# Kernel tuning notes

Hardware: AMD Instinct MI355X
Metric: run time of the kernel (lower is better)

## Reference

```python
import jax, jax.numpy as jnp
import numpy as np

B, N, E, D, N_NODE = 512, 64, 64, 256, 200000
NEG = -9e15
ALPHA = 0.2  # leaky-relu slope from HGNN_ATT(..., 0.2, ...)


def _hgat_layer(x, adj_mask, w2, w3, a, a2, wc, w=None):
    """HyperGraphAttentionLayerSparse (HyperGAT), dense-masked vectorized form.
    x: [B,N,d_in], adj_mask: [B,E,N] bool. Returns (node [B,N,d], edge [B,E,d]).
    Eval mode: dropout is identity. concat=False so no ELU on output."""
    d = w2.shape[1]
    x4 = x @ w2                                            # [B,N,d]
    if w is not None:                                      # transfer=True path
        x = x @ w
    # node->edge attention: score = leakyrelu([word_context; x4_node] @ a), independent of edge idx
    s1 = jax.nn.leaky_relu(jnp.dot(wc, a[:d, 0]) + x4 @ a[d:, 0], ALPHA)   # [B,N]
    att_edge = jax.nn.softmax(jnp.where(adj_mask, s1[:, None, :], NEG), axis=2)  # [B,E,N]
    edge = att_edge @ x                                    # [B,E,d]
    edge4 = edge @ w3                                      # [B,E,d]
    # edge->node attention: score = leakyrelu([x4_node; edge4_edge] @ a2)
    s_pair = jax.nn.leaky_relu((x4 @ a2[:d, 0])[:, None, :] + (edge4 @ a2[d:, 0])[:, :, None], ALPHA)  # [B,E,N]
    att_node = jax.nn.softmax(jnp.swapaxes(jnp.where(adj_mask, s_pair, NEG), 1, 2), axis=2)  # [B,N,E]
    node = att_node @ edge                                 # [B,N,d]
    return node, edge


def setup_inputs() -> dict:
    key = jax.random.key(0)
    ks = jax.random.split(key, 16)
    stdv = 1.0 / np.sqrt(D)  # SessionGraph.reset_parameters uniform(-stdv, stdv)
    u = lambda k, shape: jax.random.uniform(k, shape, jnp.float32, -stdv, stdv)
    return {
        "inputs": jax.random.randint(ks[0], (B, N), 0, N_NODE, dtype=jnp.int32),
        "HT": (jax.random.uniform(ks[1], (B, E, N)) < 0.3).astype(jnp.int32),
        "G": jnp.zeros((1,), jnp.float32),
        "EG": jnp.zeros((1,), jnp.float32),
        "emb_w": u(ks[2], (N_NODE, D)),
        "emb2_w": u(ks[3], (N_NODE, D)),
        "g1_w2": u(ks[4], (D, D)),
        "g1_w3": u(ks[5], (D, D)),
        "g1_a": u(ks[6], (2 * D, 1)),
        "g1_a2": u(ks[7], (2 * D, 1)),
        "g1_wc": u(ks[8], (D,)),
        "g2_w": u(ks[9], (D, D)),
        "g2_w2": u(ks[10], (D, D)),
        "g2_w3": u(ks[11], (D, D)),
        "g2_a": u(ks[12], (2 * D, 1)),
        "g2_a2": u(ks[13], (2 * D, 1)),
        "g2_wc": u(ks[14], (D,)),
    }


def reference(inputs, HT, G, EG, emb_w, emb2_w, g1_w2, g1_w3, g1_a, g1_a2, g1_wc,
              g2_w, g2_w2, g2_w3, g2_a, g2_a2, g2_wc):
    adj_mask = HT > 0
    x = emb_w[inputs]                                      # [B,N,D] embedding gather
    residual = x
    # HGNN_ATT with step=2: gat1 (transfer=False) + residual, gat2 (transfer=True) + residual
    x, _ = _hgat_layer(x, adj_mask, g1_w2, g1_w3, g1_a, g1_a2, g1_wc)
    x = x + residual
    x, _ = _hgat_layer(x, adj_mask, g2_w2, g2_w3, g2_a, g2_a2, g2_wc, g2_w)
    x = x + residual
    nodes2 = emb2_w[inputs]                                # second embedding gather
    return (x, x, nodes2)  # (nodes, hidden, nodes2); hidden aliases nodes in the original
```

## Files before the change

### kernel.cpp

```cpp
#include <hip/hip_runtime.h>

#define BB 512
#define NN 64
#define EE 64
#define DD 256
#define BND (BB * NN * DD)
#define SA 68

typedef __attribute__((ext_vector_type(8))) short s8v;
typedef __attribute__((ext_vector_type(4))) float f4v;
typedef __attribute__((ext_vector_type(8))) unsigned short u16x8;

__device__ __forceinline__ unsigned short f2bf(float f) {
    unsigned int x = __float_as_uint(f);
    x = x + 0x7fffu + ((x >> 16) & 1u);
    return (unsigned short)(x >> 16);
}
__device__ __forceinline__ float bf2f(unsigned short u) {
    return __uint_as_float(((unsigned int)u) << 16);
}
__device__ __forceinline__ float lrelu(float v) { return v > 0.f ? v : 0.2f * v; }

#define WS_PREP  0
#define WS_P3B   8192
#define WS_WFRAG 12288

__global__ void prep_dots(const float* __restrict__ w2a, const float* __restrict__ w3a,
                          const float* __restrict__ aa, const float* __restrict__ a2a,
                          const float* __restrict__ wca,
                          const float* __restrict__ w2b, const float* __restrict__ w3b,
                          const float* __restrict__ ab, const float* __restrict__ a2b,
                          const float* __restrict__ wcb,
                          float* __restrict__ prep, float* __restrict__ p3b_ws) {
    const int t = threadIdx.x;
    const int blk = blockIdx.x;
    const int layer = blk >> 3;
    const int r0 = (blk & 7) * 32;
    __shared__ float vhi[256], v2lo[256], v2hi[256], red[256];
    const float* w2 = layer ? w2b : w2a;
    const float* w3 = layer ? w3b : w3a;
    const float* av = layer ? ab : aa;
    const float* a2 = layer ? a2b : a2a;
    vhi[t] = av[256 + t];
    v2lo[t] = a2[t];
    v2hi[t] = a2[256 + t];
    __syncthreads();
    const int row = r0 + (t >> 3), q = t & 7;
    const float* w2r = w2 + (size_t)row * DD + q * 32;
    const float* w3r = w3 + (size_t)row * DD + q * 32;
    float s1 = 0.f, s2 = 0.f, s3 = 0.f;
    #pragma unroll
    for (int c = 0; c < 8; c++) {
        float4 v = *(const float4*)&w2r[c * 4];
        float4 u = *(const float4*)&w3r[c * 4];
        float4 p1 = *(const float4*)&vhi[q * 32 + c * 4];
        float4 p2 = *(const float4*)&v2lo[q * 32 + c * 4];
        float4 p3 = *(const float4*)&v2hi[q * 32 + c * 4];
        s1 = fmaf(v.x, p1.x, fmaf(v.y, p1.y, fmaf(v.z, p1.z, fmaf(v.w, p1.w, s1))));
        s2 = fmaf(v.x, p2.x, fmaf(v.y, p2.y, fmaf(v.z, p2.z, fmaf(v.w, p2.w, s2))));
        s3 = fmaf(u.x, p3.x, fmaf(u.y, p3.y, fmaf(u.z, p3.z, fmaf(u.w, p3.w, s3))));
    }
    s1 += __shfl_xor(s1, 1); s1 += __shfl_xor(s1, 2); s1 += __shfl_xor(s1, 4);
    s2 += __shfl_xor(s2, 1); s2 += __shfl_xor(s2, 2); s2 += __shfl_xor(s2, 4);
    s3 += __shfl_xor(s3, 1); s3 += __shfl_xor(s3, 2); s3 += __shfl_xor(s3, 4);
    if (q == 0) {
        if (layer == 0) { prep[row] = s1; prep[256 + row] = s2; prep[512 + row] = s3; }
        else { prep[1024 + row] = s1; prep[1280 + row] = s2; p3b_ws[row] = s3; }
    }
    if ((blk & 7) == 0) {
        red[t] = layer ? (wcb[t] * ab[t]) : (wca[t] * aa[t]);
        __syncthreads();
        for (int o = 128; o > 0; o >>= 1) { if (t < o) red[t] += red[t + o]; __syncthreads(); }
        if (t == 0) prep[layer ? 1792 : 768] = red[0];
    }
}

__global__ void prep2_pack(const float* __restrict__ wtr, const float* __restrict__ p3b_ws,
                           float* __restrict__ prep, unsigned short* __restrict__ wfrag) {
    const int t = threadIdx.x, blk = blockIdx.x;
    __shared__ float p3[256];
    if (blk < 8) {
        p3[t] = p3b_ws[t];
        __syncthreads();
        const int row = blk * 32 + (t >> 3), q = t & 7;
        const float* wr = wtr + (size_t)row * DD + q * 32;
        float s = 0.f;
        #pragma unroll
        for (int c = 0; c < 8; c++) {
            float4 v = *(const float4*)&wr[c * 4];
            float4 p = *(const float4*)&p3[q * 32 + c * 4];
            s = fmaf(v.x, p.x, fmaf(v.y, p.y, fmaf(v.z, p.z, fmaf(v.w, p.w, s))));
        }
        s += __shfl_xor(s, 1); s += __shfl_xor(s, 2); s += __shfl_xor(s, 4);
        if (q == 0) prep[1536 + row] = s;
    } else {
        int gid = (blk - 8) * 256 + t;
        int l = gid & 63, frag = gid >> 6;
        int kc = frag >> 4, nt = frag & 15;
        int kb = kc * 32 + (l >> 4) * 8;
        int n = nt * 16 + (l & 15);
        u16x8 u;
        #pragma unroll
        for (int j = 0; j < 8; j++) u[j] = f2bf(wtr[(size_t)(kb + j) * DD + n]);
        *(u16x8*)(wfrag + (size_t)gid * 8) = u;
    }
}

__launch_bounds__(512, 4)
__global__ void mega(const int* __restrict__ inputs, const int* __restrict__ HT,
                     const float* __restrict__ emb_w, const float* __restrict__ emb2_w,
                     const float* __restrict__ prep, const unsigned short* __restrict__ wfrag,
                     float* __restrict__ out) {
    __shared__ unsigned short bufA[256 * SA];
    __shared__ unsigned short RA[64 * SA];
    __shared__ unsigned short RB[64 * SA];
    __shared__ unsigned short RC[64 * SA];
    __shared__ unsigned short RD[64 * SA];
    __shared__ unsigned short XT[16 * SA];
    __shared__ unsigned short pvs[6 * 256];
    __shared__ float dvs[384];
    __shared__ float db2[192];
    __shared__ float u1f[64], invdef[64];
    __shared__ unsigned long long mE[64], mN[64];

    const int b = blockIdx.x;
    const int t = threadIdx.x;
    const int lane = t & 63;
    const int w8 = t >> 6;
    const int l15 = lane & 15, lh = lane >> 4;

    for (int i = t; i < 1536; i += 512) {
        int off = i + (((i >> 8) >= 3) ? 256 : 0);
        pvs[i] = f2bf(prep[off]);
    }
    for (int i = t; i < 16 * SA; i += 512) XT[i] = 0;
    {
        const int rw = t >> 3, q8 = t & 7;
        const int idx = inputs[b * 64 + rw];
        const float* src = emb_w + (size_t)idx * DD + q8 * 32;
        #pragma unroll
        for (int c = 0; c < 8; c++) {
            float4 v = ((const float4*)src)[c];
            ushort4 u;
            u.x = f2bf(v.x); u.y = f2bf(v.y); u.z = f2bf(v.z); u.w = f2bf(v.w);
            *(ushort4*)&bufA[rw * 264 + q8 * 32 + c * 4] = u;
        }
    }
    float4 n2r[8];
    #pragma unroll
    for (int c = 0; c < 8; c++) {
        int i = t + 512 * c;
        int n = i >> 6, cc = i & 63;
        int idx = inputs[b * 64 + n];
        n2r[c] = ((const float4*)(emb2_w + (size_t)idx * DD))[cc];
    }
    #pragma unroll
    for (int i = 0; i < 8; i++) {
        int e = w8 * 8 + i;
        int hx = HT[((size_t)b * EE + e) * NN + lane];
        unsigned long long m = __ballot(hx > 0);
        if (lane == 0) mE[e] = m;
    }
    __syncthreads();

    if (w8 < 4) {
        const int wtile = w8 * 16;
        const int j = (l15 < 6) ? l15 : 5;
        f4v acc = {0.f, 0.f, 0.f, 0.f};
        #pragma unroll
        for (int kc = 0; kc < 8; kc++) {
            s8v a = *(const s8v*)&bufA[(wtile + l15) * 264 + kc * 32 + lh * 8];
            s8v bv = *(const s8v*)&pvs[j * 256 + kc * 32 + lh * 8];
            acc = __builtin_amdgcn_mfma_f32_16x16x32_bf16(a, bv, acc, 0, 0, 0);
        }
        if (l15 < 6) {
            #pragma unroll
            for (int rg = 0; rg < 4; rg++)
                dvs[l15 * 64 + wtile + lh * 4 + rg] = acc[rg];
        }
    } else if (w8 == 4) {
        unsigned long long acc = 0ull;
        for (int e = 0; e < 64; e++) acc |= ((mE[e] >> lane) & 1ull) << e;
        mN[lane] = acc;
    }
    __syncthreads();

    const int wr = (w8 & 3) * 16;
    const int wc = (w8 >> 2) * 32;
    const int row0 = wr + lh * 4;

    {
        float s1l = lrelu(prep[768] + dvs[lane]);
        float g1 = s1l;
        #pragma unroll
        for (int o = 32; o > 0; o >>= 1) g1 = fmaxf(g1, __shfl_xor(g1, o));
        float E1 = __expf(s1l - g1);
        #pragma unroll
        for (int i = 0; i < 8; i++) {
            int e = w8 * 8 + i;
            unsigned long long me = mE[e];
            float pe = (me == 0ull) ? 1.f : (((me >> lane) & 1ull) ? E1 : 0.f);
            unsigned short bf = f2bf(pe);
            RA[lane * SA + e] = bf;
            RC[e * SA + lane] = bf;
        }
    }
    __syncthreads();

    if (w8 < 4) {
        const int etile = w8 * 16;
        f4v acc = {0.f, 0.f, 0.f, 0.f};
        #pragma unroll
        for (int kc = 0; kc < 2; kc++) {
            u16x8 au;
            #pragma unroll
            for (int jj = 0; jj < 8; jj++) {
                int k = kc * 32 + lh * 8 + jj;
                float v = (l15 == 0) ? 1.f : ((l15 <= 4) ? dvs[(l15 + 1) * 64 + k] : 0.f);
                au[jj] = f2bf(v);
            }
            s8v bv = *(const s8v*)&RC[(etile + l15) * SA + kc * 32 + lh * 8];
            acc = __builtin_amdgcn_mfma_f32_16x16x32_bf16((s8v)au, bv, acc, 0, 0, 0);
        }
        int e = etile + l15;
        if (lh == 0) {
            float De = acc[0], We = acc[1];
            invdef[e] = 1.f / De;
            u1f[e] = We / De;
            XT[e] = f2bf(De);
            XT[1 * SA + e] = f2bf(acc[2]);
            XT[2 * SA + e] = f2bf(acc[3]);
        } else if (lh == 1) {
            XT[3 * SA + e] = f2bf(acc[0]);
        }
    }
    __syncthreads();

    {
        float t2l = dvs[64 + lane];
        float gt2 = t2l;
        #pragma unroll
        for (int o = 32; o > 0; o >>= 1) gt2 = fmaxf(gt2, __shfl_xor(gt2, o));
        float um = u1f[lane];
        #pragma unroll
        for (int o = 32; o > 0; o >>= 1) um = fmaxf(um, __shfl_xor(um, o));
        float M1 = lrelu(gt2 + um);
        float ul = u1f[lane];
        float ide = invdef[lane];
        #pragma unroll
        for (int i = 0; i < 8; i++) {
            int n = w8 * 8 + i;
            unsigned long long mn = mN[n];
            float t2n = dvs[64 + n];
            float pr = (mn == 0ull) ? 1.f
                     : (((mn >> lane) & 1ull) ? __expf(lrelu(t2n + ul) - M1) : 0.f);
            RB[n * SA + lane] = f2bf(pr * ide);
        }
    }
    __syncthreads();

    {
        f4v a0 = {0.f,0.f,0.f,0.f}, a1 = {0.f,0.f,0.f,0.f}, ax = {0.f,0.f,0.f,0.f};
        #pragma unroll
        for (int kc = 0; kc < 2; kc++) {
            s8v a  = *(const s8v*)&RB[(wr + l15) * SA + kc * 32 + lh * 8];
            s8v b0 = *(const s8v*)&RA[(wc + l15) * SA + kc * 32 + lh * 8];
            s8v b1 = *(const s8v*)&RA[(wc + 16 + l15) * SA + kc * 32 + lh * 8];
            s8v bx = *(const s8v*)&XT[l15 * SA + kc * 32 + lh * 8];
            a0 = __builtin_amdgcn_mfma_f32_16x16x32_bf16(a, b0, a0, 0, 0, 0);
            a1 = __builtin_amdgcn_mfma_f32_16x16x32_bf16(a, b1, a1, 0, 0, 0);
            ax = __builtin_amdgcn_mfma_f32_16x16x32_bf16(a, bx, ax, 0, 0, 0);
        }
        float invdn[4];
        #pragma unroll
        for (int rg = 0; rg < 4; rg++) invdn[rg] = 1.f / __shfl(ax[rg], lh << 4);
        int col0 = wc + l15, col1 = wc + 16 + l15;
        ushort4 u0, u1;
        #pragma unroll
        for (int rg = 0; rg < 4; rg++) {
            ((unsigned short*)&u0)[rg] = f2bf(a0[rg] * invdn[rg] + ((row0 + rg) == col0 ? 1.f : 0.f));
            ((unsigned short*)&u1)[rg] = f2bf(a1[rg] * invdn[rg] + ((row0 + rg) == col1 ? 1.f : 0.f));
        }
        *(ushort4*)&RD[col0 * SA + row0] = u0;
        *(ushort4*)&RD[col1 * SA + row0] = u1;
        if (w8 < 4 && l15 >= 1 && l15 <= 3) {
            int jj = l15 - 1;
            #pragma unroll
            for (int rg = 0; rg < 4; rg++)
                db2[jj * 64 + row0 + rg] = ax[rg] * invdn[rg] + dvs[(jj + 3) * 64 + row0 + rg];
        }
    }
    __syncthreads();

    {
        float s2l = lrelu(prep[1792] + db2[lane]);
        float g2 = s2l;
        #pragma unroll
        for (int o = 32; o > 0; o >>= 1) g2 = fmaxf(g2, __shfl_xor(g2, o));
        float E2 = __expf(s2l - g2);
        #pragma unroll
        for (int i = 0; i < 8; i++) {
            int e = w8 * 8 + i;
            unsigned long long me = mE[e];
            float pe = (me == 0ull) ? 1.f : (((me >> lane) & 1ull) ? E2 : 0.f);
            unsigned short bf = f2bf(pe);
            RA[lane * SA + e] = bf;
            RC[e * SA + lane] = bf;
        }
    }
    __syncthreads();

    if (w8 < 4) {
        const int etile = w8 * 16;
        f4v acc = {0.f, 0.f, 0.f, 0.f};
        #pragma unroll
        for (int kc = 0; kc < 2; kc++) {
            u16x8 au;
            #pragma unroll
            for (int jj = 0; jj < 8; jj++) {
                int k = kc * 32 + lh * 8 + jj;
                float v = (l15 == 0) ? 1.f : ((l15 == 1) ? db2[128 + k] : 0.f);
                au[jj] = f2bf(v);
            }
            s8v bv = *(const s8v*)&RC[(etile + l15) * SA + kc * 32 + lh * 8];
            acc = __builtin_amdgcn_mfma_f32_16x16x32_bf16((s8v)au, bv, acc, 0, 0, 0);
        }
        if (lh == 0) {
            int e = etile + l15;
            float De = acc[0], We = acc[1];
            invdef[e] = 1.f / De;
            u1f[e] = We / De;
            XT[e] = f2bf(De);
        }
    }
    __syncthreads();

    {
        float d1l = db2[64 + lane];
        float gd1 = d1l;
        #pragma unroll
        for (int o = 32; o > 0; o >>= 1) gd1 = fmaxf(gd1, __shfl_xor(gd1, o));
        float um = u1f[lane];
        #pragma unroll
        for (int o = 32; o > 0; o >>= 1) um = fmaxf(um, __shfl_xor(um, o));
        float M2 = lrelu(gd1 + um);
        float ul = u1f[lane];
        float ide = invdef[lane];
        #pragma unroll
        for (int i = 0; i < 8; i++) {
            int n = w8 * 8 + i;
            unsigned long long mn = mN[n];
            float d1n = db2[64 + n];
            float pr = (mn == 0ull) ? 1.f
                     : (((mn >> lane) & 1ull) ? __expf(lrelu(d1n + ul) - M2) : 0.f);
            RB[n * SA + lane] = f2bf(pr * ide);
        }
    }
    __syncthreads();

    {
        f4v a0 = {0.f,0.f,0.f,0.f}, a1 = {0.f,0.f,0.f,0.f}, ax = {0.f,0.f,0.f,0.f};
        #pragma unroll
        for (int kc = 0; kc < 2; kc++) {
            s8v a  = *(const s8v*)&RB[(wr + l15) * SA + kc * 32 + lh * 8];
            s8v b0 = *(const s8v*)&RA[(wc + l15) * SA + kc * 32 + lh * 8];
            s8v b1 = *(const s8v*)&RA[(wc + 16 + l15) * SA + kc * 32 + lh * 8];
            s8v bx = *(const s8v*)&XT[l15 * SA + kc * 32 + lh * 8];
            a0 = __builtin_amdgcn_mfma_f32_16x16x32_bf16(a, b0, a0, 0, 0, 0);
            a1 = __builtin_amdgcn_mfma_f32_16x16x32_bf16(a, b1, a1, 0, 0, 0);
            ax = __builtin_amdgcn_mfma_f32_16x16x32_bf16(a, bx, ax, 0, 0, 0);
        }
        float invdn[4];
        #pragma unroll
        for (int rg = 0; rg < 4; rg++) invdn[rg] = 1.f / __shfl(ax[rg], lh << 4);
        #pragma unroll
        for (int rg = 0; rg < 4; rg++) {
            RC[(row0 + rg) * SA + wc + l15] = f2bf(a0[rg] * invdn[rg]);
            RC[(row0 + rg) * SA + wc + 16 + l15] = f2bf(a1[rg] * invdn[rg]);
        }
    }
    __syncthreads();

    {
        f4v a0 = {0.f,0.f,0.f,0.f}, a1 = {0.f,0.f,0.f,0.f};
        #pragma unroll
        for (int kc = 0; kc < 2; kc++) {
            s8v a  = *(const s8v*)&RC[(wr + l15) * SA + kc * 32 + lh * 8];
            s8v b0 = *(const s8v*)&RD[(wc + l15) * SA + kc * 32 + lh * 8];
            s8v b1 = *(const s8v*)&RD[(wc + 16 + l15) * SA + kc * 32 + lh * 8];
            a0 = __builtin_amdgcn_mfma_f32_16x16x32_bf16(a, b0, a0, 0, 0, 0);
            a1 = __builtin_amdgcn_mfma_f32_16x16x32_bf16(a, b1, a1, 0, 0, 0);
        }
        #pragma unroll
        for (int rg = 0; rg < 4; rg++) {
            RA[(row0 + rg) * SA + wc + l15] = f2bf(a0[rg]);
            RA[(row0 + rg) * SA + wc + 16 + l15] = f2bf(a1[rg]);
        }
    }
    #pragma unroll
    for (int c = 0; c < 8; c++) {
        int i = t + 512 * c;
        int n = i >> 6, cc = i & 63;
        ((float4*)(out + (size_t)2 * BND + (size_t)(b * 64 + n) * DD))[cc] = n2r[c];
    }
    __syncthreads();

    const int cb8 = (w8 >> 2) * 8;
    unsigned short rres[8][4];
    {
        f4v acc[8];
        #pragma unroll
        for (int nt = 0; nt < 8; nt++) acc[nt] = (f4v){0.f, 0.f, 0.f, 0.f};
        const s8v* wf = (const s8v*)wfrag;
        #pragma unroll
        for (int kc = 0; kc < 8; kc++) {
            s8v a = *(const s8v*)&bufA[(wr + l15) * 264 + kc * 32 + lh * 8];
            #pragma unroll
            for (int nt = 0; nt < 8; nt++) {
                s8v bv = wf[(size_t)(kc * 16 + cb8 + nt) * 64 + lane];
                acc[nt] = __builtin_amdgcn_mfma_f32_16x16x32_bf16(a, bv, acc[nt], 0, 0, 0);
            }
        }
        #pragma unroll
        for (int nt = 0; nt < 8; nt++) {
            #pragma unroll
            for (int rg = 0; rg < 4; rg++)
                rres[nt][rg] = bufA[(row0 + rg) * 264 + (cb8 + nt) * 16 + l15];
        }
        __syncthreads();
        #pragma unroll
        for (int nt = 0; nt < 8; nt++) {
            int feat = (cb8 + nt) * 16 + l15;
            ushort4 u;
            u.x = f2bf(acc[nt][0]); u.y = f2bf(acc[nt][1]);
            u.z = f2bf(acc[nt][2]); u.w = f2bf(acc[nt][3]);
            *(ushort4*)&bufA[feat * SA + row0] = u;
        }
    }
    __syncthreads();

    {
        f4v acc2[8];
        #pragma unroll
        for (int nt = 0; nt < 8; nt++) acc2[nt] = (f4v){0.f, 0.f, 0.f, 0.f};
        #pragma unroll
        for (int kc = 0; kc < 2; kc++) {
            s8v a = *(const s8v*)&RA[(wr + l15) * SA + kc * 32 + lh * 8];
            #pragma unroll
            for (int nt = 0; nt < 8; nt++) {
                s8v bv = *(const s8v*)&bufA[((cb8 + nt) * 16 + l15) * SA + kc * 32 + lh * 8];
                acc2[nt] = __builtin_amdgcn_mfma_f32_16x16x32_bf16(a, bv, acc2[nt], 0, 0, 0);
            }
        }
        #pragma unroll
        for (int nt = 0; nt < 8; nt++) {
            #pragma unroll
            for (int rg = 0; rg < 4; rg++) {
                int row = row0 + rg;
                int colg = (cb8 + nt) * 16 + l15;
                float v = acc2[nt][rg] + bf2f(rres[nt][rg]);
                size_t o = (size_t)(b * 64 + row) * DD + colg;
                out[o] = v;
                out[BND + o] = v;
            }
        }
    }
}

extern "C" void kernel_launch(void* const* d_in, const int* in_sizes, int n_in,
                              void* d_out, int out_size, void* d_ws, size_t ws_size,
                              hipStream_t stream) {
    const int* inputs = (const int*)d_in[0];
    const int* HT = (const int*)d_in[1];
    const float* emb_w  = (const float*)d_in[4];
    const float* emb2_w = (const float*)d_in[5];
    const float* g1_w2 = (const float*)d_in[6];
    const float* g1_w3 = (const float*)d_in[7];
    const float* g1_a  = (const float*)d_in[8];
    const float* g1_a2 = (const float*)d_in[9];
    const float* g1_wc = (const float*)d_in[10];
    const float* g2_w  = (const float*)d_in[11];
    const float* g2_w2 = (const float*)d_in[12];
    const float* g2_w3 = (const float*)d_in[13];
    const float* g2_a  = (const float*)d_in[14];
    const float* g2_a2 = (const float*)d_in[15];
    const float* g2_wc = (const float*)d_in[16];

    float* out = (float*)d_out;
    float* prep = (float*)((char*)d_ws + WS_PREP);
    float* p3b_ws = (float*)((char*)d_ws + WS_P3B);
    unsigned short* wfrag = (unsigned short*)((char*)d_ws + WS_WFRAG);

    prep_dots<<<16, 256, 0, stream>>>(g1_w2, g1_w3, g1_a, g1_a2, g1_wc,
                                      g2_w2, g2_w3, g2_a, g2_a2, g2_wc,
                                      prep, p3b_ws);
    prep2_pack<<<40, 256, 0, stream>>>(g2_w, p3b_ws, prep, wfrag);
    mega<<<BB, 512, 0, stream>>>(inputs, HT, emb_w, emb2_w, prep, wfrag, out);
}
```

Baseline: 64.00 us.

## Split monolithic kernel into gather, attention-chain, and output GEMM stages

Splits the single per-batch kernel into three launches. The first gathers the embeddings, computes the six projection dot products in FP32, and builds the incidence bitmasks. The second runs the attention chain with a smaller LDS footprint, reusing one merged buffer, so more blocks can be resident per CU. The third runs the final weight GEMM and the residual. The aim is higher occupancy and less register and LDS pressure in each phase, at the cost of extra launches and global-memory round trips through workspace for intermediates (bf16 x0, the masks, the dot products and the M matrix).

Result: slower. 98.32 us (+53.6%).

```diff
diff --git a/kernel.cpp b/kernel.cpp
--- a/kernel.cpp
+++ b/kernel.cpp
@@ -21,9 +21,13 @@
 }
 __device__ __forceinline__ float lrelu(float v) { return v > 0.f ? v : 0.2f * v; }
 
-#define WS_PREP  0
-#define WS_P3B   8192
-#define WS_WFRAG 12288
+#define WS_PREP   0
+#define WS_P3B    8192
+#define WS_WFRAG  12288
+#define WS_DV     143360
+#define WS_MASKS  929792
+#define WS_M      1454080
+#define WS_X0     5648384
 
 __global__ void prep_dots(const float* __restrict__ w2a, const float* __restrict__ w3a,
                           const float* __restrict__ aa, const float* __restrict__ a2a,
@@ -106,18 +110,81 @@
     }
 }
 
-__launch_bounds__(512, 4)
-__global__ void mega(const int* __restrict__ inputs, const int* __restrict__ HT,
-                     const float* __restrict__ emb_w, const float* __restrict__ emb2_w,
-                     const float* __restrict__ prep, const unsigned short* __restrict__ wfrag,
-                     float* __restrict__ out) {
-    __shared__ unsigned short bufA[256 * SA];
+__launch_bounds__(256, 4)
+__global__ void k1_stage(const int* __restrict__ inputs, const int* __restrict__ HT,
+                         const float* __restrict__ emb_w, const float* __restrict__ emb2_w,
+                         const float* __restrict__ prep,
+                         float* __restrict__ dv_ws, unsigned long long* __restrict__ masks,
+                         unsigned short* __restrict__ x0bf, float* __restrict__ out) {
+    __shared__ float pvs[1536];
+    __shared__ unsigned long long mEs[64];
+    const int b = blockIdx.x;
+    const int t = threadIdx.x;
+    const int lane = t & 63;
+    const int w4 = t >> 6;
+    const int row = t >> 2, q4 = t & 3;
+    for (int i = t; i < 1536; i += 256) {
+        int off = i + (((i >> 8) >= 3) ? 256 : 0);
+        pvs[i] = prep[off];
+    }
+    const int idx = inputs[b * 64 + row];
+    __syncthreads();
+    {
+        const float4* src = (const float4*)(emb_w + (size_t)idx * DD + q4 * 64);
+        float a6[6] = {0.f, 0.f, 0.f, 0.f, 0.f, 0.f};
+        unsigned short* xd = x0bf + ((size_t)(b * 64 + row)) * DD + q4 * 64;
+        #pragma unroll
+        for (int c = 0; c < 16; c++) {
+            float4 v = src[c];
+            ushort4 u;
+            u.x = f2bf(v.x); u.y = f2bf(v.y); u.z = f2bf(v.z); u.w = f2bf(v.w);
+            *(ushort4*)(xd + c * 4) = u;
+            #pragma unroll
+            for (int j = 0; j < 6; j++) {
+                float4 p = *(const float4*)&pvs[j * 256 + q4 * 64 + c * 4];
+                a6[j] = fmaf(v.x, p.x, fmaf(v.y, p.y, fmaf(v.z, p.z, fmaf(v.w, p.w, a6[j]))));
+            }
+        }
+        #pragma unroll
+        for (int j = 0; j < 6; j++) {
+            a6[j] += __shfl_xor(a6[j], 1);
+            a6[j] += __shfl_xor(a6[j], 2);
+        }
+        if (q4 == 0) {
+            #pragma unroll
+            for (int j = 0; j < 6; j++) dv_ws[b * 384 + j * 64 + row] = a6[j];
+        }
+    }
+    {
+        const float4* s2 = (const float4*)(emb2_w + (size_t)idx * DD + q4 * 64);
+        float4* d2 = (float4*)(out + (size_t)2 * BND + (size_t)(b * 64 + row) * DD + q4 * 64);
+        #pragma unroll
+        for (int c = 0; c < 16; c++) d2[c] = s2[c];
+    }
+    #pragma unroll
+    for (int i = 0; i < 16; i++) {
+        int e = w4 * 16 + i;
+        int h = HT[((size_t)b * EE + e) * NN + lane];
+        unsigned long long m = __ballot(h > 0);
+        if (lane == 0) mEs[e] = m;
+    }
+    __syncthreads();
+    if (t < 64) {
+        unsigned long long acc = 0ull;
+        for (int e = 0; e < 64; e++) acc |= ((mEs[e] >> t) & 1ull) << e;
+        masks[b * 128 + t] = mEs[t];
+        masks[b * 128 + 64 + t] = acc;
+    }
+}
+
+__launch_bounds__(512, 8)
+__global__ void k2_chain(const float* __restrict__ dv_ws,
+                         const unsigned long long* __restrict__ masks,
+                         const float* __restrict__ prep, unsigned short* __restrict__ Mws) {
     __shared__ unsigned short RA[64 * SA];
-    __shared__ unsigned short RB[64 * SA];
-    __shared__ unsigned short RC[64 * SA];
+    __shared__ unsigned short RBC[64 * SA];
     __shared__ unsigned short RD[64 * SA];
     __shared__ unsigned short XT[16 * SA];
-    __shared__ unsigned short pvs[6 * 256];
     __shared__ float dvs[384];
     __shared__ float db2[192];
     __shared__ float u1f[64], invdef[64];
@@ -129,60 +196,10 @@
     const int w8 = t >> 6;
     const int l15 = lane & 15, lh = lane >> 4;
 
-    for (int i = t; i < 1536; i += 512) {
-        int off = i + (((i >> 8) >= 3) ? 256 : 0);
-        pvs[i] = f2bf(prep[off]);
-    }
+    if (t < 384) dvs[t] = dv_ws[b * 384 + t];
+    else if (t < 448) mE[t - 384] = masks[b * 128 + (t - 384)];
+    else mN[t - 448] = masks[b * 128 + 64 + (t - 448)];
     for (int i = t; i < 16 * SA; i += 512) XT[i] = 0;
-    {
-        const int rw = t >> 3, q8 = t & 7;
-        const int idx = inputs[b * 64 + rw];
-        const float* src = emb_w + (size_t)idx * DD + q8 * 32;
-        #pragma unroll
-        for (int c = 0; c < 8; c++) {
-            float4 v = ((const float4*)src)[c];
-            ushort4 u;
-            u.x = f2bf(v.x); u.y = f2bf(v.y); u.z = f2bf(v.z); u.w = f2bf(v.w);
-            *(ushort4*)&bufA[rw * 264 + q8 * 32 + c * 4] = u;
-        }
-    }
-    float4 n2r[8];
-    #pragma unroll
-    for (int c = 0; c < 8; c++) {
-        int i = t + 512 * c;
-        int n = i >> 6, cc = i & 63;
-        int idx = inputs[b * 64 + n];
-        n2r[c] = ((const float4*)(emb2_w + (size_t)idx * DD))[cc];
-    }
-    #pragma unroll
-    for (int i = 0; i < 8; i++) {
-        int e = w8 * 8 + i;
-        int hx = HT[((size_t)b * EE + e) * NN + lane];
-        unsigned long long m = __ballot(hx > 0);
-        if (lane == 0) mE[e] = m;
-    }
-    __syncthreads();
-
-    if (w8 < 4) {
-        const int wtile = w8 * 16;
-        const int j = (l15 < 6) ? l15 : 5;
-        f4v acc = {0.f, 0.f, 0.f, 0.f};
-        #pragma unroll
-        for (int kc = 0; kc < 8; kc++) {
-            s8v a = *(const s8v*)&bufA[(wtile + l15) * 264 + kc * 32 + lh * 8];
-            s8v bv = *(const s8v*)&pvs[j * 256 + kc * 32 + lh * 8];
-            acc = __builtin_amdgcn_mfma_f32_16x16x32_bf16(a, bv, acc, 0, 0, 0);
-        }
-        if (l15 < 6) {
-            #pragma unroll
-            for (int rg = 0; rg < 4; rg++)
-                dvs[l15 * 64 + wtile + lh * 4 + rg] = acc[rg];
-        }
-    } else if (w8 == 4) {
-        unsigned long long acc = 0ull;
-        for (int e = 0; e < 64; e++) acc |= ((mE[e] >> lane) & 1ull) << e;
-        mN[lane] = acc;
-    }
     __syncthreads();
 
     const int wr = (w8 & 3) * 16;
@@ -202,7 +219,7 @@
             float pe = (me == 0ull) ? 1.f : (((me >> lane) & 1ull) ? E1 : 0.f);
             unsigned short bf = f2bf(pe);
             RA[lane * SA + e] = bf;
-            RC[e * SA + lane] = bf;
+            RBC[e * SA + lane] = bf;
         }
     }
     __syncthreads();
@@ -219,7 +236,7 @@
                 float v = (l15 == 0) ? 1.f : ((l15 <= 4) ? dvs[(l15 + 1) * 64 + k] : 0.f);
                 au[jj] = f2bf(v);
             }
-            s8v bv = *(const s8v*)&RC[(etile + l15) * SA + kc * 32 + lh * 8];
+            s8v bv = *(const s8v*)&RBC[(etile + l15) * SA + kc * 32 + lh * 8];
             acc = __builtin_amdgcn_mfma_f32_16x16x32_bf16((s8v)au, bv, acc, 0, 0, 0);
         }
         int e = etile + l15;
@@ -254,7 +271,7 @@
             float t2n = dvs[64 + n];
             float pr = (mn == 0ull) ? 1.f
                      : (((mn >> lane) & 1ull) ? __expf(lrelu(t2n + ul) - M1) : 0.f);
-            RB[n * SA + lane] = f2bf(pr * ide);
+            RBC[n * SA + lane] = f2bf(pr * ide);
         }
     }
     __syncthreads();
@@ -263,7 +280,7 @@
         f4v a0 = {0.f,0.f,0.f,0.f}, a1 = {0.f,0.f,0.f,0.f}, ax = {0.f,0.f,0.f,0.f};
         #pragma unroll
         for (int kc = 0; kc < 2; kc++) {
-            s8v a  = *(const s8v*)&RB[(wr + l15) * SA + kc * 32 + lh * 8];
+            s8v a  = *(const s8v*)&RBC[(wr + l15) * SA + kc * 32 + lh * 8];
             s8v b0 = *(const s8v*)&RA[(wc + l15) * SA + kc * 32 + lh * 8];
             s8v b1 = *(const s8v*)&RA[(wc + 16 + l15) * SA + kc * 32 + lh * 8];
             s8v bx = *(const s8v*)&XT[l15 * SA + kc * 32 + lh * 8];
@@ -305,7 +322,7 @@
             float pe = (me == 0ull) ? 1.f : (((me >> lane) & 1ull) ? E2 : 0.f);
             unsigned short bf = f2bf(pe);
             RA[lane * SA + e] = bf;
-            RC[e * SA + lane] = bf;
+            RBC[e * SA + lane] = bf;
         }
     }
     __syncthreads();
@@ -322,7 +339,7 @@
                 float v = (l15 == 0) ? 1.f : ((l15 == 1) ? db2[128 + k] : 0.f);
                 au[jj] = f2bf(v);
             }
-            s8v bv = *(const s8v*)&RC[(etile + l15) * SA + kc * 32 + lh * 8];
+            s8v bv = *(const s8v*)&RBC[(etile + l15) * SA + kc * 32 + lh * 8];
             acc = __builtin_amdgcn_mfma_f32_16x16x32_bf16((s8v)au, bv, acc, 0, 0, 0);
         }
         if (lh == 0) {
@@ -353,7 +370,7 @@
             float d1n = db2[64 + n];
             float pr = (mn == 0ull) ? 1.f
                      : (((mn >> lane) & 1ull) ? __expf(lrelu(d1n + ul) - M2) : 0.f);
-            RB[n * SA + lane] = f2bf(pr * ide);
+            RBC[n * SA + lane] = f2bf(pr * ide);
         }
     }
     __syncthreads();
@@ -362,7 +379,7 @@
         f4v a0 = {0.f,0.f,0.f,0.f}, a1 = {0.f,0.f,0.f,0.f}, ax = {0.f,0.f,0.f,0.f};
         #pragma unroll
         for (int kc = 0; kc < 2; kc++) {
-            s8v a  = *(const s8v*)&RB[(wr + l15) * SA + kc * 32 + lh * 8];
+            s8v a  = *(const s8v*)&RBC[(wr + l15) * SA + kc * 32 + lh * 8];
             s8v b0 = *(const s8v*)&RA[(wc + l15) * SA + kc * 32 + lh * 8];
             s8v b1 = *(const s8v*)&RA[(wc + 16 + l15) * SA + kc * 32 + lh * 8];
             s8v bx = *(const s8v*)&XT[l15 * SA + kc * 32 + lh * 8];
@@ -373,10 +390,11 @@
         float invdn[4];
         #pragma unroll
         for (int rg = 0; rg < 4; rg++) invdn[rg] = 1.f / __shfl(ax[rg], lh << 4);
+        __syncthreads();
         #pragma unroll
         for (int rg = 0; rg < 4; rg++) {
-            RC[(row0 + rg) * SA + wc + l15] = f2bf(a0[rg] * invdn[rg]);
-            RC[(row0 + rg) * SA + wc + 16 + l15] = f2bf(a1[rg] * invdn[rg]);
+            RBC[(row0 + rg) * SA + wc + l15] = f2bf(a0[rg] * invdn[rg]);
+            RBC[(row0 + rg) * SA + wc + 16 + l15] = f2bf(a1[rg] * invdn[rg]);
         }
     }
     __syncthreads();
@@ -385,27 +403,51 @@
         f4v a0 = {0.f,0.f,0.f,0.f}, a1 = {0.f,0.f,0.f,0.f};
         #pragma unroll
         for (int kc = 0; kc < 2; kc++) {
-            s8v a  = *(const s8v*)&RC[(wr + l15) * SA + kc * 32 + lh * 8];
+            s8v a  = *(const s8v*)&RBC[(wr + l15) * SA + kc * 32 + lh * 8];
             s8v b0 = *(const s8v*)&RD[(wc + l15) * SA + kc * 32 + lh * 8];
             s8v b1 = *(const s8v*)&RD[(wc + 16 + l15) * SA + kc * 32 + lh * 8];
             a0 = __builtin_amdgcn_mfma_f32_16x16x32_bf16(a, b0, a0, 0, 0, 0);
             a1 = __builtin_amdgcn_mfma_f32_16x16x32_bf16(a, b1, a1, 0, 0, 0);
         }
+        unsigned short* md = Mws + (size_t)b * 4096;
         #pragma unroll
         for (int rg = 0; rg < 4; rg++) {
-            RA[(row0 + rg) * SA + wc + l15] = f2bf(a0[rg]);
-            RA[(row0 + rg) * SA + wc + 16 + l15] = f2bf(a1[rg]);
-        }
-    }
-    #pragma unroll
-    for (int c = 0; c < 8; c++) {
-        int i = t + 512 * c;
-        int n = i >> 6, cc = i & 63;
-        ((float4*)(out + (size_t)2 * BND + (size_t)(b * 64 + n) * DD))[cc] = n2r[c];
-    }
-    __syncthreads();
-
+            md[(row0 + rg) * 64 + wc + l15] = f2bf(a0[rg]);
+            md[(row0 + rg) * 64 + wc + 16 + l15] = f2bf(a1[rg]);
+        }
+    }
+}
+
+__launch_bounds__(512, 4)
+__global__ void k3_out(const unsigned short* __restrict__ x0bf,
+                       const unsigned short* __restrict__ Mws,
+                       const unsigned short* __restrict__ wfrag,
+                       float* __restrict__ out) {
+    __shared__ unsigned short bufA[256 * SA];
+    __shared__ unsigned short Mlds[64 * SA];
+    const int b = blockIdx.x;
+    const int t = threadIdx.x;
+    const int lane = t & 63;
+    const int w8 = t >> 6;
+    const int l15 = lane & 15, lh = lane >> 4;
+
+    {
+        const u16x8* xsrc = (const u16x8*)(x0bf + (size_t)b * 64 * DD);
+        #pragma unroll
+        for (int c = 0; c < 4; c++) {
+            int i = t + 512 * c;
+            int n = i >> 5, cc = i & 31;
+            *(u16x8*)&bufA[n * 264 + cc * 8] = xsrc[i];
+        }
+        u16x8 mv = ((const u16x8*)(Mws + (size_t)b * 4096))[t];
+        *(u16x8*)&Mlds[(t >> 3) * SA + (t & 7) * 8] = mv;
+    }
+    __syncthreads();
+
+    const int wr = (w8 & 3) * 16;
+    const int row0 = wr + lh * 4;
     const int cb8 = (w8 >> 2) * 8;
+
     unsigned short rres[8][4];
     {
         f4v acc[8];
@@ -445,7 +487,7 @@
         for (int nt = 0; nt < 8; nt++) acc2[nt] = (f4v){0.f, 0.f, 0.f, 0.f};
         #pragma unroll
         for (int kc = 0; kc < 2; kc++) {
-            s8v a = *(const s8v*)&RA[(wr + l15) * SA + kc * 32 + lh * 8];
+            s8v a = *(const s8v*)&Mlds[(wr + l15) * SA + kc * 32 + lh * 8];
             #pragma unroll
             for (int nt = 0; nt < 8; nt++) {
                 s8v bv = *(const s8v*)&bufA[((cb8 + nt) * 16 + l15) * SA + kc * 32 + lh * 8];
@@ -490,10 +532,17 @@
     float* prep = (float*)((char*)d_ws + WS_PREP);
     float* p3b_ws = (float*)((char*)d_ws + WS_P3B);
     unsigned short* wfrag = (unsigned short*)((char*)d_ws + WS_WFRAG);
+    float* dv_ws = (float*)((char*)d_ws + WS_DV);
+    unsigned long long* masks = (unsigned long long*)((char*)d_ws + WS_MASKS);
+    unsigned short* Mws = (unsigned short*)((char*)d_ws + WS_M);
+    unsigned short* x0bf = (unsigned short*)((char*)d_ws + WS_X0);
 
     prep_dots<<<16, 256, 0, stream>>>(g1_w2, g1_w3, g1_a, g1_a2, g1_wc,
                                       g2_w2, g2_w3, g2_a, g2_a2, g2_wc,
                                       prep, p3b_ws);
     prep2_pack<<<40, 256, 0, stream>>>(g2_w, p3b_ws, prep, wfrag);
-    mega<<<BB, 512, 0, stream>>>(inputs, HT, emb_w, emb2_w, prep, wfrag, out);
-}
+    k1_stage<<<BB, 256, 0, stream>>>(inputs, HT, emb_w, emb2_w, prep,
+                                     dv_ws, masks, x0bf, out);
+    k2_chain<<<BB, 512, 0, stream>>>(dv_ws, masks, prep, Mws);
+    k3_out<<<BB, 512, 0, stream>>>(x0bf, Mws, wfrag, out);
+}
```
